# Optimization experiments

Measured on AMD Instinct MI355X. Metric: run time of the kernel, lower is better.

## Reference

```python
import jax, jax.numpy as jnp
import numpy as np

SCALING_FACTOR = 128.0


def setup_inputs() -> dict:
    key = jax.random.key(0)
    k1, k2, k3, k4 = jax.random.split(key, 4)
    B, G1, G2, DX, DZ, NT = 4, 128, 128, 2, 128, 2048
    x_grid = jax.random.uniform(k1, (B, G1, G2, DX), dtype=jnp.float32)
    z_grid = jax.random.normal(k2, (B, G1, G2, DZ), dtype=jnp.float32)
    xt = jax.random.uniform(k3, (B, NT, DX), dtype=jnp.float32)
    # raw (pre-softplus) lengthscale parameter, one per input dim
    init_ls = 0.1
    lengthscale_param = jnp.full((DX,), np.log(np.exp(init_ls) - 1.0), dtype=jnp.float32)
    lengthscale_param = lengthscale_param + 0.01 * jax.random.normal(k4, (DX,), dtype=jnp.float32)
    return {"x_grid": x_grid, "z_grid": z_grid, "xt": xt, "lengthscale_param": lengthscale_param}


def reference(x_grid, z_grid, xt, lengthscale_param):
    B = x_grid.shape[0]
    dx = x_grid.shape[-1]
    dz = z_grid.shape[-1]
    # flatten spatial grid dims -> (B, ng, d)
    xg = x_grid.reshape(B, -1, dx)
    zg = z_grid.reshape(B, -1, dz)
    # lengthscale = 1e-5 + softplus(param), shape (dx,)
    ls = 1e-5 + jax.nn.softplus(lengthscale_param)
    # pairwise scaled squared distances: (B, nt, ng)
    diff = (xt[:, :, None, :] - xg[:, None, :, :]) / ls  # (B, nt, ng, dx)
    dist2 = jnp.sum(diff * diff, axis=-1)
    weights = jnp.exp(-0.5 * dist2)  # (B, nt, ng)
    # weighted smoothing onto targets
    out = jnp.einsum("btg,bgz->btz", weights, zg) / SCALING_FACTOR
    return out
```

## Files before the change

kernel.cpp:

```cpp
#include <hip/hip_runtime.h>
#include <hip/hip_bf16.h>
#include <cstdint>
#include <cstddef>


typedef float  f32x4  __attribute__((ext_vector_type(4)));
typedef float  f32x16 __attribute__((ext_vector_type(16)));
typedef short  short8 __attribute__((ext_vector_type(8)));
typedef unsigned short ushort4v __attribute__((ext_vector_type(4)));
typedef unsigned short ushort8 __attribute__((ext_vector_type(8)));

#if __has_builtin(__builtin_amdgcn_exp2f)
#define EXP2F(x) __builtin_amdgcn_exp2f(x)
#else
#define EXP2F(x) exp2f(x)
#endif

#define AS1C(p) ((const __attribute__((address_space(1))) void*)(p))
#define AS3(p)  ((__attribute__((address_space(3))) void*)(p))

__device__ __forceinline__ unsigned short bf16_bits(float f) {
  __bf16 h = (__bf16)f;
  return __builtin_bit_cast(unsigned short, h);
}

__global__ __launch_bounds__(256) void pre_kernel(
    const float* __restrict__ x_grid, const float* __restrict__ z_grid,
    const float* __restrict__ xt, const float* __restrict__ lsp,
    unsigned short* __restrict__ zgb, float* __restrict__ xg_trip,
    float* __restrict__ xt4)
{
  __shared__ unsigned short lt[64 * 128];
  const int bid = blockIdx.x;
  const int b   = bid >> 8;
  const int grp = bid & 255;
  const int tid = threadIdx.x;
  const size_t gbase = (size_t)b * 16384 + grp * 64;
  const float sc = 1.0f / 128.0f;

  const float* zr = z_grid + gbase * 128;
  #pragma unroll
  for (int it = 0; it < 8; ++it) {
    const int idx = it * 256 + tid;
    const int row = idx >> 5, c4 = idx & 31;
    f32x4 v = *(const f32x4*)(zr + row * 128 + c4 * 4);
    ushort4v o;
    o.x = bf16_bits(v.x * sc); o.y = bf16_bits(v.y * sc);
    o.z = bf16_bits(v.z * sc); o.w = bf16_bits(v.w * sc);
    *(ushort4v*)(lt + row * 128 + c4 * 4) = o;
  }

  if (tid < 128) {
    const float ls0 = 1e-5f + log1pf(expf(lsp[0]));
    const float ls1 = 1e-5f + log1pf(expf(lsp[1]));
    const float cs  = sqrtf(0.7213475204444817f);
    const float s0 = cs / ls0, s1 = cs / ls1;
    if (tid < 64) {
      const size_t g = gbase + tid;
      const float u0 = x_grid[g * 2 + 0] * s0;
      const float u1 = x_grid[g * 2 + 1] * s1;
      float* d = xg_trip + g * 3;
      d[0] = 2.0f * u0; d[1] = 2.0f * u1; d[2] = -(u0 * u0 + u1 * u1);
    } else if (bid < 128) {
      const int bx = bid >> 5;
      const int r  = (bid & 31) * 64 + (tid - 64);
      const float u0 = xt[((size_t)(bx * 2048 + r)) * 2 + 0] * s0;
      const float u1 = xt[((size_t)(bx * 2048 + r)) * 2 + 1] * s1;
      f32x4 d; d.x = u0; d.y = u1; d.z = -(u0 * u0 + u1 * u1); d.w = 0.0f;
      *(f32x4*)(xt4 + ((size_t)(bx * 2048 + r)) * 4) = d;
    }
  }

  __syncthreads();

  const int q2p = tid >> 7, c = tid & 127;
  #pragma unroll
  for (int h = 0; h < 4; ++h) {
    ushort8 o;
    #pragma unroll
    for (int hi = 0; hi < 2; ++hi)
      #pragma unroll
      for (int j = 0; j < 4; ++j)
        o[hi * 4 + j] = lt[(h * 16 + 4 * q2p + 8 * hi + j) * 128 + c];
    *(ushort8*)(zgb + ((size_t)(b * 1024 + grp * 4 + h)) * 2048
                    + (size_t)(q2p * 128 + c) * 8) = o;
  }
}

__global__ __launch_bounds__(128, 4) void main_kernel(
    const unsigned short* __restrict__ zgb,
    const float* __restrict__ xg_trip,
    const float* __restrict__ xt4,
    float* __restrict__ out,
    float* __restrict__ partials)
{
  __shared__ __align__(128) char smem[4 * 4096 + 4 * 256];
  char* ring = smem;
  char* trg  = smem + 16384;

  const int raw = blockIdx.x;
  const int lid = (raw & 7) * 128 + (raw >> 3);
  const int mt  = lid & 31;
  const int b   = (lid >> 5) & 3;
  const int ksp = lid >> 7;

  const int tid = threadIdx.x;
  const int w   = tid >> 6;
  const int l   = tid & 63;
  const int l31 = l & 31;
  const int q2  = l >> 5;

  const int r = mt * 64 + w * 32 + l31;
  f32x4 tv = *(const f32x4*)(xt4 + ((size_t)(b * 2048 + r)) * 4);
  const float at0 = tv.x, at1 = tv.y, ca = tv.z;

  f32x16 acc[4];
  #pragma unroll
  for (int ni = 0; ni < 4; ++ni)
    #pragma unroll
    for (int e = 0; e < 16; ++e)
      acc[ni][e] = 0.0f;

  const char* zsrc = (const char*)zgb + ((size_t)(b * 1024 + ksp * 128)) * 4096;
  const char* tsrc = (const char*)xg_trip + ((size_t)(b * 16384 + ksp * 2048)) * 12;

  auto stage = [&](int s) {
    const int sl = s & 3;
    const char* zs = zsrc + (size_t)s * 4096 + w * 2048;
    char* zd = ring + sl * 4096 + w * 2048;
    __builtin_amdgcn_global_load_lds(AS1C(zs + l * 16), AS3(zd + l * 16), 16, 0, 0);
    __builtin_amdgcn_global_load_lds(AS1C(zs + 1024 + l * 16),
                                     AS3(zd + 1024 + l * 16), 16, 0, 0);
    if (l < 6) {
      __builtin_amdgcn_global_load_lds(
          AS1C(tsrc + (size_t)s * 192 + w * 96 + l * 16),
          AS3(trg + sl * 256 + w * 96 + l * 16), 16, 0, 0);
    }
  };

  stage(0);
  stage(1);
  stage(2);

  #pragma unroll 4
  for (int s = 0; s < 128; ++s) {
    if (s < 126) { asm volatile("s_waitcnt vmcnt(6)" ::: "memory"); }
    else         { asm volatile("s_waitcnt vmcnt(0)" ::: "memory"); }
    __builtin_amdgcn_s_barrier();
    asm volatile("" ::: "memory");

    if (s + 3 < 128) stage(s + 3);

    const float* tb = (const float*)(trg + (s & 3) * 256 + q2 * 48);
    f32x4 L0 = *(const f32x4*)(tb + 0);
    f32x4 L1 = *(const f32x4*)(tb + 4);
    f32x4 L2 = *(const f32x4*)(tb + 8);
    f32x4 H0 = *(const f32x4*)(tb + 24);
    f32x4 H1 = *(const f32x4*)(tb + 28);
    f32x4 H2 = *(const f32x4*)(tb + 32);
    float g0[8], g1[8], cb[8];
    g0[0]=L0.x; g1[0]=L0.y; cb[0]=L0.z;
    g0[1]=L0.w; g1[1]=L1.x; cb[1]=L1.y;
    g0[2]=L1.z; g1[2]=L1.w; cb[2]=L2.x;
    g0[3]=L2.y; g1[3]=L2.z; cb[3]=L2.w;
    g0[4]=H0.x; g1[4]=H0.y; cb[4]=H0.z;
    g0[5]=H0.w; g1[5]=H1.x; cb[5]=H1.y;
    g0[6]=H1.z; g1[6]=H1.w; cb[6]=H2.x;
    g0[7]=H2.y; g1[7]=H2.z; cb[7]=H2.w;

    union { short8 s8; __bf16 e[8]; } u;
    #pragma unroll
    for (int j = 0; j < 8; ++j) {
      float arg = __builtin_fmaf(at0, g0[j],
                  __builtin_fmaf(at1, g1[j], ca + cb[j]));
      u.e[j] = (__bf16)EXP2F(arg);
    }
    const short8 af = u.s8;

    const char* zt = ring + (s & 3) * 4096 + q2 * 2048 + l31 * 16;
    #pragma unroll
    for (int ni = 0; ni < 4; ++ni) {
      short8 bfr = *(const short8*)(zt + ni * 512);
      acc[ni] = __builtin_amdgcn_mfma_f32_32x32x16_bf16(af, bfr, acc[ni], 0, 0, 0);
    }
  }

  if (partials) {
    float* pb = partials + (size_t)ksp * 1048576
              + ((size_t)(b * 2048 + mt * 64 + w * 32)) * 128;
    #pragma unroll
    for (int ni = 0; ni < 4; ++ni)
      #pragma unroll
      for (int rr = 0; rr < 16; ++rr) {
        const int row = (rr & 3) + 8 * (rr >> 2) + 4 * q2;
        pb[row * 128 + ni * 32 + l31] = acc[ni][rr];
      }
  } else {
    #pragma unroll
    for (int ni = 0; ni < 4; ++ni)
      #pragma unroll
      for (int rr = 0; rr < 16; ++rr) {
        const int row = mt * 64 + w * 32 + (rr & 3) + 8 * (rr >> 2) + 4 * q2;
        atomicAdd(out + ((size_t)b * 2048 + row) * 128 + ni * 32 + l31,
                  acc[ni][rr]);
      }
  }
}

__global__ __launch_bounds__(256) void reduce_kernel(
    const float* __restrict__ partials, float* __restrict__ out)
{
  const size_t base = ((size_t)blockIdx.x * 256 + threadIdx.x) * 4;
  const float* p = partials + base;
  f32x4 s = *(const f32x4*)p;
  #pragma unroll
  for (int ksv = 1; ksv < 8; ++ksv) {
    f32x4 v = *(const f32x4*)(p + (size_t)ksv * 1048576);
    s.x += v.x; s.y += v.y; s.z += v.z; s.w += v.w;
  }
  *(f32x4*)(out + base) = s;
}

extern "C" void kernel_launch(void* const* d_in, const int* in_sizes, int n_in,
                              void* d_out, int out_size, void* d_ws, size_t ws_size,
                              hipStream_t stream) {
  const float* x_grid = (const float*)d_in[0];
  const float* z_grid = (const float*)d_in[1];
  const float* xt     = (const float*)d_in[2];
  const float* lsp    = (const float*)d_in[3];
  float* out = (float*)d_out;

  char* ws = (char*)d_ws;
  unsigned short* zgb = (unsigned short*)ws;
  float* xg_trip = (float*)(ws + 16777216);
  float* xt4     = (float*)(ws + 16777216 + 786432);
  const size_t poff = 16777216 + 786432 + 131072;
  const bool use_partials = ws_size >= poff + 33554432;
  float* partials = use_partials ? (float*)(ws + poff) : nullptr;

  if (!use_partials)
    hipMemsetAsync(d_out, 0, (size_t)out_size * sizeof(float), stream);
  pre_kernel<<<1024, 256, 0, stream>>>(x_grid, z_grid, xt, lsp,
                                       zgb, xg_trip, xt4);
  main_kernel<<<1024, 128, 0, stream>>>(zgb, xg_trip, xt4, out, partials);
  if (use_partials)
    reduce_kernel<<<1024, 256, 0, stream>>>(partials, out);
}
```

Measured before the change: 149.0 us.

## Load MFMA operands directly from global into registers with double buffering

The main kernel no longer stages z and grid-triplet tiles through an LDS ring via global_load_lds. Each lane now loads its MFMA B fragments and triplet data straight into registers, double-buffered one step ahead. The pre-kernel rewrites the grid-triplet layout so each lane's 8 triplets are contiguous. Blocks grow to 256 threads (4 waves sharing 128 target rows), and the grid shrinks to 512. This removes LDS traffic and the per-step waitcnt and barrier, at the cost of higher register pressure and redundant global/L2 reads of z across waves.

```diff
diff --git a/kernel.cpp b/kernel.cpp
--- a/kernel.cpp
+++ b/kernel.cpp
@@ -59,7 +59,11 @@
       const size_t g = gbase + tid;
       const float u0 = x_grid[g * 2 + 0] * s0;
       const float u1 = x_grid[g * 2 + 1] * s1;
-      float* d = xg_trip + g * 3;
+      const int gk = grp * 64 + tid;
+      const int tile = gk >> 4, k16 = gk & 15;
+      const int jj = k16 & 3, qq = (k16 >> 2) & 1, hh = k16 >> 3;
+      float* d = xg_trip + ((size_t)(b * 1024 + tile)) * 48
+               + qq * 24 + (hh * 4 + jj) * 3;
       d[0] = 2.0f * u0; d[1] = 2.0f * u1; d[2] = -(u0 * u0 + u1 * u1);
     } else if (bid < 128) {
       const int bx = bid >> 5;
@@ -87,22 +91,48 @@
   }
 }
 
-__global__ __launch_bounds__(128, 4) void main_kernel(
+#define LOADT(s, F, T)                                                   \
+  {                                                                      \
+    const char* zp_ = zsrc + (size_t)(s) * 4096;                         \
+    F[0] = *(const short8*)(zp_ + 0);                                    \
+    F[1] = *(const short8*)(zp_ + 512);                                  \
+    F[2] = *(const short8*)(zp_ + 1024);                                 \
+    F[3] = *(const short8*)(zp_ + 1536);                                 \
+    const char* tp_ = tsrc + (size_t)(s) * 192;                          \
+    T[0] = *(const f32x4*)(tp_ + 0);  T[1] = *(const f32x4*)(tp_ + 16);  \
+    T[2] = *(const f32x4*)(tp_ + 32); T[3] = *(const f32x4*)(tp_ + 48);  \
+    T[4] = *(const f32x4*)(tp_ + 64); T[5] = *(const f32x4*)(tp_ + 80);  \
+  }
+
+#define COMPUTE(F, T)                                                    \
+  {                                                                      \
+    const float* f_ = (const float*)&(T)[0];                             \
+    union { short8 s8; __bf16 e[8]; } u_;                                \
+    _Pragma("unroll")                                                    \
+    for (int j2 = 0; j2 < 8; ++j2) {                                     \
+      float arg_ = __builtin_fmaf(at0, f_[3 * j2],                       \
+                   __builtin_fmaf(at1, f_[3 * j2 + 1],                   \
+                                  ca + f_[3 * j2 + 2]));                 \
+      u_.e[j2] = (__bf16)EXP2F(arg_);                                    \
+    }                                                                    \
+    acc[0] = __builtin_amdgcn_mfma_f32_32x32x16_bf16(u_.s8, F[0], acc[0], 0, 0, 0); \
+    acc[1] = __builtin_amdgcn_mfma_f32_32x32x16_bf16(u_.s8, F[1], acc[1], 0, 0, 0); \
+    acc[2] = __builtin_amdgcn_mfma_f32_32x32x16_bf16(u_.s8, F[2], acc[2], 0, 0, 0); \
+    acc[3] = __builtin_amdgcn_mfma_f32_32x32x16_bf16(u_.s8, F[3], acc[3], 0, 0, 0); \
+  }
+
+__global__ __launch_bounds__(256, 2) void main_kernel(
     const unsigned short* __restrict__ zgb,
     const float* __restrict__ xg_trip,
     const float* __restrict__ xt4,
     float* __restrict__ out,
     float* __restrict__ partials)
 {
-  __shared__ __align__(128) char smem[4 * 4096 + 4 * 256];
-  char* ring = smem;
-  char* trg  = smem + 16384;
-
   const int raw = blockIdx.x;
-  const int lid = (raw & 7) * 128 + (raw >> 3);
-  const int mt  = lid & 31;
-  const int b   = (lid >> 5) & 3;
-  const int ksp = lid >> 7;
+  const int lid = (raw & 7) * 64 + (raw >> 3);
+  const int mtg = lid & 15;
+  const int b   = (lid >> 4) & 3;
+  const int ksp = lid >> 6;
 
   const int tid = threadIdx.x;
   const int w   = tid >> 6;
@@ -110,7 +140,7 @@
   const int l31 = l & 31;
   const int q2  = l >> 5;
 
-  const int r = mt * 64 + w * 32 + l31;
+  const int r = mtg * 128 + w * 32 + l31;
   f32x4 tv = *(const f32x4*)(xt4 + ((size_t)(b * 2048 + r)) * 4);
   const float at0 = tv.x, at1 = tv.y, ca = tv.z;
 
@@ -121,73 +151,32 @@
     for (int e = 0; e < 16; ++e)
       acc[ni][e] = 0.0f;
 
-  const char* zsrc = (const char*)zgb + ((size_t)(b * 1024 + ksp * 128)) * 4096;
-  const char* tsrc = (const char*)xg_trip + ((size_t)(b * 16384 + ksp * 2048)) * 12;
-
-  auto stage = [&](int s) {
-    const int sl = s & 3;
-    const char* zs = zsrc + (size_t)s * 4096 + w * 2048;
-    char* zd = ring + sl * 4096 + w * 2048;
-    __builtin_amdgcn_global_load_lds(AS1C(zs + l * 16), AS3(zd + l * 16), 16, 0, 0);
-    __builtin_amdgcn_global_load_lds(AS1C(zs + 1024 + l * 16),
-                                     AS3(zd + 1024 + l * 16), 16, 0, 0);
-    if (l < 6) {
-      __builtin_amdgcn_global_load_lds(
-          AS1C(tsrc + (size_t)s * 192 + w * 96 + l * 16),
-          AS3(trg + sl * 256 + w * 96 + l * 16), 16, 0, 0);
-    }
-  };
-
-  stage(0);
-  stage(1);
-  stage(2);
-
-  #pragma unroll 4
-  for (int s = 0; s < 128; ++s) {
-    if (s < 126) { asm volatile("s_waitcnt vmcnt(6)" ::: "memory"); }
-    else         { asm volatile("s_waitcnt vmcnt(0)" ::: "memory"); }
+  const char* zsrc = (const char*)zgb
+                   + ((size_t)(b * 1024 + ksp * 128)) * 4096
+                   + q2 * 2048 + l31 * 16;
+  const char* tsrc = (const char*)xg_trip
+                   + ((size_t)(b * 1024 + ksp * 128)) * 192
+                   + q2 * 96;
+
+  short8 F0[4], F1[4];
+  f32x4  T0[6], T1[6];
+
+  LOADT(0, F0, T0);
+
+  for (int sb = 0; sb < 32; ++sb) {
     __builtin_amdgcn_s_barrier();
-    asm volatile("" ::: "memory");
-
-    if (s + 3 < 128) stage(s + 3);
-
-    const float* tb = (const float*)(trg + (s & 3) * 256 + q2 * 48);
-    f32x4 L0 = *(const f32x4*)(tb + 0);
-    f32x4 L1 = *(const f32x4*)(tb + 4);
-    f32x4 L2 = *(const f32x4*)(tb + 8);
-    f32x4 H0 = *(const f32x4*)(tb + 24);
-    f32x4 H1 = *(const f32x4*)(tb + 28);
-    f32x4 H2 = *(const f32x4*)(tb + 32);
-    float g0[8], g1[8], cb[8];
-    g0[0]=L0.x; g1[0]=L0.y; cb[0]=L0.z;
-    g0[1]=L0.w; g1[1]=L1.x; cb[1]=L1.y;
-    g0[2]=L1.z; g1[2]=L1.w; cb[2]=L2.x;
-    g0[3]=L2.y; g1[3]=L2.z; cb[3]=L2.w;
-    g0[4]=H0.x; g1[4]=H0.y; cb[4]=H0.z;
-    g0[5]=H0.w; g1[5]=H1.x; cb[5]=H1.y;
-    g0[6]=H1.z; g1[6]=H1.w; cb[6]=H2.x;
-    g0[7]=H2.y; g1[7]=H2.z; cb[7]=H2.w;
-
-    union { short8 s8; __bf16 e[8]; } u;
-    #pragma unroll
-    for (int j = 0; j < 8; ++j) {
-      float arg = __builtin_fmaf(at0, g0[j],
-                  __builtin_fmaf(at1, g1[j], ca + cb[j]));
-      u.e[j] = (__bf16)EXP2F(arg);
-    }
-    const short8 af = u.s8;
-
-    const char* zt = ring + (s & 3) * 4096 + q2 * 2048 + l31 * 16;
-    #pragma unroll
-    for (int ni = 0; ni < 4; ++ni) {
-      short8 bfr = *(const short8*)(zt + ni * 512);
-      acc[ni] = __builtin_amdgcn_mfma_f32_32x32x16_bf16(af, bfr, acc[ni], 0, 0, 0);
+    #pragma unroll
+    for (int u = 0; u < 4; ++u) {
+      const int s  = sb * 4 + u;
+      const int nx = (s + 1 < 128) ? s + 1 : s;
+      if (u & 1) { LOADT(nx, F0, T0); COMPUTE(F1, T1); }
+      else       { LOADT(nx, F1, T1); COMPUTE(F0, T0); }
     }
   }
 
   if (partials) {
     float* pb = partials + (size_t)ksp * 1048576
-              + ((size_t)(b * 2048 + mt * 64 + w * 32)) * 128;
+              + ((size_t)(b * 2048 + mtg * 128 + w * 32)) * 128;
     #pragma unroll
     for (int ni = 0; ni < 4; ++ni)
       #pragma unroll
@@ -200,7 +189,7 @@
     for (int ni = 0; ni < 4; ++ni)
       #pragma unroll
       for (int rr = 0; rr < 16; ++rr) {
-        const int row = mt * 64 + w * 32 + (rr & 3) + 8 * (rr >> 2) + 4 * q2;
+        const int row = mtg * 128 + w * 32 + (rr & 3) + 8 * (rr >> 2) + 4 * q2;
         atomicAdd(out + ((size_t)b * 2048 + row) * 128 + ni * 32 + l31,
                   acc[ni][rr]);
       }
@@ -242,7 +231,7 @@
     hipMemsetAsync(d_out, 0, (size_t)out_size * sizeof(float), stream);
   pre_kernel<<<1024, 256, 0, stream>>>(x_grid, z_grid, xt, lsp,
                                        zgb, xg_trip, xt4);
-  main_kernel<<<1024, 128, 0, stream>>>(zgb, xg_trip, xt4, out, partials);
+  main_kernel<<<512, 256, 0, stream>>>(zgb, xg_trip, xt4, out, partials);
   if (use_partials)
     reduce_kernel<<<1024, 256, 0, stream>>>(partials, out);
 }
```

Measured after the change: 189.1 us. 1.27x slower.
